# Performance work log

Hardware: AMD Instinct MI355X
Metric: run time of the kernel (lower is better)

The kernel has to match this reference:

```python
import jax, jax.numpy as jnp
import numpy as np
import math

D_MODEL = 2048
N_HEADS = 16
D_FF = 8192
SEQ = 2048
BATCH = 2
THETA = 10000.0
EPS = 1e-5


def _rope(x, pos):
    # x: [B, H, S, d_k] ; pos: [B, S] int
    d = x.shape[-1]
    inv_freq = 1.0 / (THETA ** (jnp.arange(0, d, 2, dtype=jnp.float32) / d))  # [d/2]
    ang = pos[..., None].astype(jnp.float32) * inv_freq  # [B, S, d/2]
    cos = jnp.cos(ang)[:, None, :, :, None]  # [B,1,S,d/2,1]
    sin = jnp.sin(ang)[:, None, :, :, None]
    xr = x.reshape(*x.shape[:-1], d // 2, 2)
    x1, x2 = xr[..., 0], xr[..., 1]
    rot = jnp.stack((-x2, x1), axis=-1)  # rotate pairs
    out = xr * cos + rot * sin
    return out.reshape(x.shape)


def _trunc_normal(key, shape, in_f, out_f):
    std = math.sqrt(2.0 / (in_f + out_f))
    return jax.random.truncated_normal(key, -3.0, 3.0, shape, jnp.float32) * std


def setup_inputs() -> dict:
    key = jax.random.key(0)
    ks = jax.random.split(key, 8)
    x = jax.random.normal(ks[0], (BATCH, SEQ, D_MODEL), jnp.float32)
    token_positions = jnp.sort(jax.random.randint(ks[1], (BATCH, SEQ), 0, SEQ), axis=-1)
    W_qkv = _trunc_normal(ks[2], (3 * D_MODEL, D_MODEL), D_MODEL, 3 * D_MODEL)
    W_o = _trunc_normal(ks[3], (D_MODEL, D_MODEL), D_MODEL, D_MODEL)
    W1 = _trunc_normal(ks[4], (D_FF, D_MODEL), D_MODEL, D_FF)
    W3 = _trunc_normal(ks[5], (D_FF, D_MODEL), D_MODEL, D_FF)
    W2 = _trunc_normal(ks[6], (D_MODEL, D_FF), D_FF, D_MODEL)
    g1 = jnp.ones((D_MODEL,), jnp.float32)
    g2 = jnp.ones((D_MODEL,), jnp.float32)
    return {"x": x, "token_positions": token_positions, "W_qkv": W_qkv, "W_o": W_o,
            "g1": g1, "g2": g2, "W1": W1, "W3": W3, "W2": W2}


def _rmsnorm(x, g):
    xf = x.astype(jnp.float32)
    rms = jnp.sqrt(jnp.mean(xf * xf, axis=-1, keepdims=True) + EPS)
    return (xf / rms * g).astype(x.dtype)


def reference(x, token_positions, W_qkv, W_o, g1, g2, W1, W3, W2):
    B, S, D = x.shape
    H = N_HEADS
    dk = D // H
    # --- attention sublayer ---
    h = _rmsnorm(x, g1)
    qkv = jnp.einsum('bsi,oi->bso', h, W_qkv)  # [B,S,3D]
    q, k, v = jnp.split(qkv, 3, axis=-1)
    to_heads = lambda t: t.reshape(B, S, H, dk).transpose(0, 2, 1, 3)  # [B,H,S,dk]
    q, k, v = to_heads(q), to_heads(k), to_heads(v)
    q = _rope(q, token_positions)
    k = _rope(k, token_positions)
    scores = jnp.einsum('bhnd,bhmd->bhnm', q, k) / math.sqrt(dk)  # [B,H,S,S]
    mask = jnp.tril(jnp.ones((S, S), dtype=bool))
    scores = jnp.where(mask, scores, -jnp.inf)
    attn = jax.nn.softmax(scores, axis=-1)
    o = jnp.einsum('bhnm,bhmd->bhnd', attn, v)
    o = o.transpose(0, 2, 1, 3).reshape(B, S, D)
    x = x + jnp.einsum('bsi,oi->bso', o, W_o)
    # --- SwiGLU FFN sublayer ---
    h2 = _rmsnorm(x, g2)
    x1 = jnp.einsum('bsi,oi->bso', h2, W1)
    x3 = jnp.einsum('bsi,oi->bso', h2, W3)
    x = x + jnp.einsum('bsi,oi->bso', jax.nn.silu(x1) * x3, W2)
    return x
```

## Files before the change

### kernel.cpp

```cpp
#include <hip/hip_runtime.h>

#define DEV __device__ __forceinline__

typedef __bf16 bf16x8 __attribute__((ext_vector_type(8)));
typedef float f32x4 __attribute__((ext_vector_type(4)));
typedef unsigned short u16x8 __attribute__((ext_vector_type(8)));

DEV unsigned short f2bf(float f) {
  unsigned int u = __float_as_uint(f);
  u += 0x7fffu + ((u >> 16) & 1u);
  return (unsigned short)(u >> 16);
}
DEV float bf2f(unsigned short h) {
  return __uint_as_float(((unsigned int)h) << 16);
}
DEV void gload16(const void* g, void* l) {
  __builtin_amdgcn_global_load_lds(
      (const __attribute__((address_space(1))) unsigned int*)g,
      (__attribute__((address_space(3))) unsigned int*)l, 16, 0, 0);
}
DEV f32x4 mfma16(bf16x8 a, bf16x8 b, f32x4 c) {
  return __builtin_amdgcn_mfma_f32_16x16x32_bf16(a, b, c, 0, 0, 0);
}

#define SB   __builtin_amdgcn_s_barrier()
#define SCH  __builtin_amdgcn_sched_barrier(0)
#define LGKM0 asm volatile("s_waitcnt lgkmcnt(0)" ::: "memory")
#define LGKM4 asm volatile("s_waitcnt lgkmcnt(4)" ::: "memory")
#define VM6  asm volatile("s_waitcnt vmcnt(6)" ::: "memory")
#define PRIO1 __builtin_amdgcn_s_setprio(1)
#define PRIO0 __builtin_amdgcn_s_setprio(0)

__global__ __launch_bounds__(256) void k_cvt(const float* __restrict__ in,
                                             unsigned short* __restrict__ out, int n8) {
  const int stride = gridDim.x * 256;
  for (int i = blockIdx.x * 256 + threadIdx.x; i < n8; i += stride) {
    const float4* p = (const float4*)(in + (long)i * 8);
    const float4 a = p[0], b = p[1];
    u16x8 o = { f2bf(a.x), f2bf(a.y), f2bf(a.z), f2bf(a.w),
                f2bf(b.x), f2bf(b.y), f2bf(b.z), f2bf(b.w) };
    *(u16x8*)(out + (long)i * 8) = o;
  }
}

__global__ __launch_bounds__(256) void k_add(float* __restrict__ out,
                                             const float* __restrict__ p, int n4) {
  const int stride = gridDim.x * 256;
  for (int i = blockIdx.x * 256 + threadIdx.x; i < n4; i += stride) {
    float4 a = ((const float4*)out)[i];
    const float4 b = ((const float4*)p)[i];
    a.x += b.x; a.y += b.y; a.z += b.z; a.w += b.w;
    ((float4*)out)[i] = a;
  }
}

__global__ __launch_bounds__(256) void k_rmsnorm(const float* __restrict__ x,
                                                 const float* __restrict__ g,
                                                 unsigned short* __restrict__ out) {
  const int row = blockIdx.x;
  const int t = threadIdx.x;
  const float4* xr = (const float4*)(x + (long)row * 2048);
  const float4 a = xr[t * 2], c = xr[t * 2 + 1];
  float ss = a.x * a.x + a.y * a.y + a.z * a.z + a.w * a.w +
             c.x * c.x + c.y * c.y + c.z * c.z + c.w * c.w;
#pragma unroll
  for (int o = 32; o > 0; o >>= 1) ss += __shfl_down(ss, o);
  __shared__ float ws4[4];
  __shared__ float invs;
  if ((t & 63) == 0) ws4[t >> 6] = ss;
  __syncthreads();
  if (t == 0) invs = 1.0f / sqrtf((ws4[0] + ws4[1] + ws4[2] + ws4[3]) * (1.0f / 2048.0f) + 1e-5f);
  __syncthreads();
  const float inv = invs;
  const float4* gr = (const float4*)g;
  const float4 g0 = gr[t * 2], g1v = gr[t * 2 + 1];
  u16x8 o8 = { f2bf(a.x * inv * g0.x),  f2bf(a.y * inv * g0.y),
               f2bf(a.z * inv * g0.z),  f2bf(a.w * inv * g0.w),
               f2bf(c.x * inv * g1v.x), f2bf(c.y * inv * g1v.y),
               f2bf(c.z * inv * g1v.z), f2bf(c.w * inv * g1v.w) };
  *(u16x8*)(out + (long)row * 2048 + t * 8) = o8;
}

__global__ __launch_bounds__(256) void k_rmsnorm2(const float* __restrict__ xa,
                                                  const float* __restrict__ xb,
                                                  const float* __restrict__ g,
                                                  float* __restrict__ xsum,
                                                  unsigned short* __restrict__ out) {
  const int row = blockIdx.x;
  const int t = threadIdx.x;
  const float4* ar = (const float4*)(xa + (long)row * 2048);
  const float4* br = (const float4*)(xb + (long)row * 2048);
  float4 a = ar[t * 2], c = ar[t * 2 + 1];
  const float4 pa = br[t * 2], pc = br[t * 2 + 1];
  a.x += pa.x; a.y += pa.y; a.z += pa.z; a.w += pa.w;
  c.x += pc.x; c.y += pc.y; c.z += pc.z; c.w += pc.w;
  float4* sr = (float4*)(xsum + (long)row * 2048);
  sr[t * 2] = a; sr[t * 2 + 1] = c;
  float ss = a.x * a.x + a.y * a.y + a.z * a.z + a.w * a.w +
             c.x * c.x + c.y * c.y + c.z * c.z + c.w * c.w;
#pragma unroll
  for (int o = 32; o > 0; o >>= 1) ss += __shfl_down(ss, o);
  __shared__ float ws4[4];
  __shared__ float invs;
  if ((t & 63) == 0) ws4[t >> 6] = ss;
  __syncthreads();
  if (t == 0) invs = 1.0f / sqrtf((ws4[0] + ws4[1] + ws4[2] + ws4[3]) * (1.0f / 2048.0f) + 1e-5f);
  __syncthreads();
  const float inv = invs;
  const float4* gr = (const float4*)g;
  const float4 g0 = gr[t * 2], g1v = gr[t * 2 + 1];
  u16x8 o8 = { f2bf(a.x * inv * g0.x),  f2bf(a.y * inv * g0.y),
               f2bf(a.z * inv * g0.z),  f2bf(a.w * inv * g0.w),
               f2bf(c.x * inv * g1v.x), f2bf(c.y * inv * g1v.y),
               f2bf(c.z * inv * g1v.z), f2bf(c.w * inv * g1v.w) };
  *(u16x8*)(out + (long)row * 2048 + t * 8) = o8;
}

template <int EPI>
__global__ __launch_bounds__(512, 2) void k_gemm256(
    const unsigned short* __restrict__ A, const unsigned short* __restrict__ B,
    unsigned short* __restrict__ outBF, float* __restrict__ outF,
    const float* __restrict__ resid, const unsigned short* __restrict__ aux,
    float* __restrict__ partial, const int* __restrict__ tp,
    unsigned short* __restrict__ p2, unsigned short* __restrict__ p3,
    int M, int N, int K, int Keff) {
  __shared__ __align__(16) unsigned short lds[2][2][2][128][64];
  const int tid = threadIdx.x;
  const int wid = tid >> 6, lane = tid & 63;
  const int wr = wid >> 2, wc = wid & 3;
  const int fr = lane & 15, g4 = lane >> 4;

  const int nwg = gridDim.x;
  int bid = blockIdx.x;
  { int q = nwg >> 3, r = nwg & 7, xcd = bid & 7, lo = bid >> 3;
    bid = (xcd < r ? xcd * (q + 1) : r * (q + 1) + (xcd - r) * q) + lo; }
  int tile = bid, ks = 0;
  if constexpr (EPI == 3) { ks = bid & 1; tile = bid >> 1; }
  const int nxb = N >> 8;
  const int bx = tile % nxb, by = tile / nxb;
  const int arow0 = by << 8, bcol0 = bx << 8;
  const int NT = Keff >> 6;

  const int srow = tid >> 3;
  const int sg = (tid & 7) ^ (srow & 7);
  const unsigned short* Asrc = A + (long)(arow0 + srow) * K + (long)ks * Keff + (sg << 3);
  const unsigned short* Bsrc = B + (long)(bcol0 + srow) * K + (long)ks * Keff + (sg << 3);

  const int posk0 = (g4 ^ (lane & 7)) << 3;
  const int posk1 = ((4 + g4) ^ (lane & 7)) << 3;

  f32x4 acc[8][4] = {};
  bf16x8 a[4][2], b0[2][2], b1[2][2];

#define STAGE(SRC, xs, bufi, mat, h)                                            \
  { const unsigned short* s_ = (SRC) + (long)(h) * 128 * K + (long)(xs) * 64;   \
    unsigned short* d_ = &lds[bufi][mat][h][0][0] + wid * 512;                  \
    gload16(s_, d_);                                                            \
    gload16(s_ + (long)64 * K, d_ + 4096); }
#define RD_A(BA, mh)                                                            \
  _Pragma("unroll") for (int m_ = 0; m_ < 4; ++m_) {                            \
    const unsigned short* p_ = (BA) + ((mh) * 64 + m_ * 16 + fr) * 64;          \
    a[m_][0] = *(const bf16x8*)(p_ + posk0);                                    \
    a[m_][1] = *(const bf16x8*)(p_ + posk1); }
#define RD_B(BB, arr, nh)                                                       \
  _Pragma("unroll") for (int n_ = 0; n_ < 2; ++n_) {                            \
    const unsigned short* p_ = (BB) + ((nh) * 32 + n_ * 16 + fr) * 64;          \
    arr[n_][0] = *(const bf16x8*)(p_ + posk0);                                  \
    arr[n_][1] = *(const bf16x8*)(p_ + posk1); }
#define MM(mh, nh, Bv)                                                          \
  _Pragma("unroll") for (int k_ = 0; k_ < 2; ++k_)                              \
  _Pragma("unroll") for (int m_ = 0; m_ < 4; ++m_)                              \
  _Pragma("unroll") for (int n_ = 0; n_ < 2; ++n_)                              \
    acc[(mh)*4+m_][(nh)*2+n_] = mfma16(a[m_][k_], Bv[n_][k_], acc[(mh)*4+m_][(nh)*2+n_]);

  STAGE(Asrc, 0, 0, 0, 0);
  STAGE(Asrc, 0, 0, 0, 1);
  STAGE(Bsrc, 0, 0, 1, 0);
  STAGE(Bsrc, 0, 0, 1, 1);
  { const int x1p = (NT > 1) ? 1 : 0;
    STAGE(Bsrc, x1p, 1, 1, 0);
    STAGE(Bsrc, x1p, 1, 1, 1);
    STAGE(Asrc, x1p, 1, 0, 0); }
  VM6; SCH; SB; SCH;
  {
    const unsigned short* baseA = &lds[0][0][wr][0][0];
    const unsigned short* baseB = &lds[0][1][wc >> 1][0][0] + (wc & 1) * 4096;
    RD_A(baseA, 0); RD_B(baseB, b0, 0);
  }

  for (int t = 0; t < NT; ++t) {
    const unsigned short* baseA = &lds[t & 1][0][wr][0][0];
    const unsigned short* baseB = &lds[t & 1][1][wc >> 1][0][0] + (wc & 1) * 4096;
    const unsigned short* baseA2 = &lds[(t + 1) & 1][0][wr][0][0];
    const unsigned short* baseB2 = &lds[(t + 1) & 1][1][wc >> 1][0][0] + (wc & 1) * 4096;
    const int x1 = (t + 1 < NT) ? t + 1 : NT - 1;
    const int x2i = (t + 2 < NT) ? t + 2 : NT - 1;
    const int bn = (t + 1) & 1, bc = t & 1;

    SB;
    RD_B(baseB, b1, 1);
    STAGE(Asrc, x1, bn, 0, 1);
    LGKM4; SCH;
    PRIO1; MM(0, 0, b0); PRIO0;
    LGKM0; SCH;
    PRIO1; MM(0, 1, b1); PRIO0;

    SB;
    RD_A(baseA, 1);
    STAGE(Bsrc, x2i, bc, 1, 0);
    LGKM0; SCH;
    PRIO1; MM(1, 1, b1); PRIO0;

    SB;
    STAGE(Asrc, x2i, bc, 0, 0);
    STAGE(Bsrc, x2i, bc, 1, 1);
    PRIO1; MM(1, 0, b0); PRIO0;
    VM6; SCH; SB; SCH;
    RD_A(baseA2, 0);
    RD_B(baseB2, b0, 0);
  }
#undef STAGE
#undef RD_A
#undef RD_B
#undef MM

  const int er = g4 << 2;
  if constexpr (EPI == 4) {
    const int region = bcol0 >> 11;
#pragma unroll
    for (int m = 0; m < 8; ++m) {
      const int grow = arow0 + wr * 128 + m * 16 + er;
      float pos4[4];
#pragma unroll
      for (int r = 0; r < 4; ++r)
        pos4[r] = (region < 2) ? (float)tp[grow + r] : 0.f;
#pragma unroll
      for (int n = 0; n < 4; ++n) {
        const int gcol = bcol0 + wc * 64 + n * 16 + fr;
        const int d = gcol & 127;
        const float invf = __expf((float)(d >> 1) * -0.14391156831212787f);
        const int h = (gcol >> 7) & 15;
#pragma unroll
        for (int r = 0; r < 4; ++r) {
          const int row = grow + r;
          const int b = row >> 11, s = row & 2047;
          float v = acc[m][n][r];
          if (region < 2) {
            const float other = __shfl_xor(v, 1);
            float cc, sn;
            __sincosf(pos4[r] * invf, &sn, &cc);
            v = (d & 1) ? (v * cc + other * sn) : (v * cc - other * sn);
          }
          unsigned short* dst = (region == 0) ? outBF : (region == 1 ? p2 : p3);
          dst[((long)((b << 4) + h) * 2048 + s) * 128 + d] = f2bf(v);
        }
      }
    }
  } else {
#pragma unroll
    for (int m = 0; m < 8; ++m) {
#pragma unroll
      for (int n = 0; n < 4; ++n) {
        const int grow = arow0 + wr * 128 + m * 16 + er;
        const int gcol = bcol0 + wc * 64 + n * 16 + fr;
#pragma unroll
        for (int r = 0; r < 4; ++r) {
          const long idx = (long)(grow + r) * N + gcol;
          const float v = acc[m][n][r];
          if constexpr (EPI == 0) {
            outBF[idx] = f2bf(v);
          } else if constexpr (EPI == 1) {
            outF[idx] = resid[idx] + v;
          } else if constexpr (EPI == 2) {
            const float x1v = bf2f(aux[idx]);
            const float sl = x1v / (1.0f + __expf(-x1v));
            outBF[idx] = f2bf(sl * v);
          } else {
            if (ks == 0) outF[idx] = resid[idx] + v;
            else         partial[idx] = v;
          }
        }
      }
    }
  }
}

__global__ __launch_bounds__(256) void k_vtrans(const unsigned short* __restrict__ Vh,
                                                unsigned short* __restrict__ Vt, int S) {
  __shared__ __align__(16) unsigned short t[128 * 72];
  const int bh = blockIdx.x;
  const int s0 = blockIdx.y << 6;
  const int tid = threadIdx.x;
  const int sl = tid >> 2, c4 = tid & 3;
#pragma unroll
  for (int it = 0; it < 4; ++it) {
    const int chunk = c4 * 4 + it;
    u16x8 v = *(const u16x8*)(Vh + ((long)bh * S + s0 + sl) * 128 + chunk * 8);
#pragma unroll
    for (int jj = 0; jj < 8; ++jj) t[(chunk * 8 + jj) * 72 + sl] = v[jj];
  }
  __syncthreads();
  const int d = tid >> 1, half = tid & 1;
  unsigned short* dst = Vt + ((long)bh * 128 + d) * S + s0 + half * 32;
  const unsigned short* srcr = &t[d * 72 + half * 32];
#pragma unroll
  for (int u = 0; u < 4; ++u)
    *(u16x8*)(dst + u * 8) = *(const u16x8*)(srcr + u * 8);
}

__global__ __launch_bounds__(256) void k_attn(const unsigned short* __restrict__ Q,
                                              const unsigned short* __restrict__ Kh,
                                              const unsigned short* __restrict__ Vt,
                                              unsigned short* __restrict__ O, int S) {
  __shared__ __align__(16) unsigned short lds_k[64 * 128];
  __shared__ __align__(16) unsigned short lds_v[128 * 64];
  __shared__ __align__(16) unsigned short lds_p[4 * 16 * 64];
  const int bh = blockIdx.x;
  const int b = bh >> 4, h = bh & 15;
  const int qt = gridDim.y - 1 - blockIdx.y;
  const int q0 = qt << 6;
  const int tid = threadIdx.x, w = tid >> 6, lane = tid & 63;
  const int fr = lane & 15, g4 = lane >> 4;

  bf16x8 qf[4];
  {
    const unsigned short* qb = Q + ((long)bh * S + q0 + w * 16 + fr) * 128 + (g4 << 3);
#pragma unroll
    for (int kk = 0; kk < 4; ++kk) qf[kk] = *(const bf16x8*)(qb + kk * 32);
  }

  f32x4 accO[8] = {};
  float mrow[4], lrow[4];
#pragma unroll
  for (int r = 0; r < 4; ++r) { mrow[r] = -1e30f; lrow[r] = 0.f; }

  const int k_row = (w << 4) + g4;
  const int k_cb = fr << 4;
  const int v_row = (w << 5) + (lane >> 3);
  const int v_cb = (lane & 7) << 4;
  const long kbase = (long)bh * S * 128;
  const long vbase = (long)bh * 128 * S;

  const int ntile = qt + 1;
  for (int it = 0; it < ntile; ++it) {
    const int kv0 = it << 6;
#pragma unroll
    for (int j = 0; j < 4; ++j) {
      const int kr = k_row + j * 4;
      const int kc = k_cb ^ ((kr & 7) << 4);
      gload16(Kh + kbase + (long)(kv0 + kr) * 128 + (kc >> 1), &lds_k[w * 2048 + j * 512]);
      const int vr = v_row + j * 8;
      const int vc = v_cb ^ ((vr & 7) << 4);
      gload16(Vt + vbase + (long)vr * S + kv0 + (vc >> 1), &lds_v[w * 2048 + j * 512]);
    }
    __syncthreads();

    f32x4 sc[4] = {};
#pragma unroll
    for (int kk = 0; kk < 4; ++kk) {
      const int kb = (kk << 6) + (g4 << 4);
#pragma unroll
      for (int n = 0; n < 4; ++n) {
        const int krw = n * 16 + fr;
        const int swz = (krw & 7) << 4;
        bf16x8 kf = *(const bf16x8*)&lds_k[krw * 128 + ((kb ^ swz) >> 1)];
        sc[n] = mfma16(qf[kk], kf, sc[n]);
      }
    }

    const float scl = 0.08838834764831845f;
    float sv[4][4];
    const bool needmask = (kv0 + 63 > q0 + w * 16);
#pragma unroll
    for (int n = 0; n < 4; ++n)
#pragma unroll
      for (int r = 0; r < 4; ++r) {
        float v = sc[n][r] * scl;
        if (needmask) {
          const int qi = q0 + w * 16 + (g4 << 2) + r;
          const int ki = kv0 + n * 16 + fr;
          if (ki > qi) v = -1e30f;
        }
        sv[n][r] = v;
      }
    float corr[4];
#pragma unroll
    for (int r = 0; r < 4; ++r) {
      float tm = fmaxf(fmaxf(sv[0][r], sv[1][r]), fmaxf(sv[2][r], sv[3][r]));
      tm = fmaxf(tm, __shfl_xor(tm, 1));
      tm = fmaxf(tm, __shfl_xor(tm, 2));
      tm = fmaxf(tm, __shfl_xor(tm, 4));
      tm = fmaxf(tm, __shfl_xor(tm, 8));
      const float mn = fmaxf(mrow[r], tm);
      corr[r] = __expf(mrow[r] - mn);
      mrow[r] = mn;
    }
    float rs[4] = {0.f, 0.f, 0.f, 0.f};
#pragma unroll
    for (int n = 0; n < 4; ++n)
#pragma unroll
      for (int r = 0; r < 4; ++r) {
        const float p = __expf(sv[n][r] - mrow[r]);
        rs[r] += p;
        const int pr = (g4 << 2) + r;
        const int pc = (n * 16 + fr) << 1;
        lds_p[(w << 10) + pr * 64 + ((pc ^ ((pr & 7) << 4)) >> 1)] = f2bf(p);
      }
#pragma unroll
    for (int r = 0; r < 4; ++r) {
      float s = rs[r];
      s += __shfl_xor(s, 1);
      s += __shfl_xor(s, 2);
      s += __shfl_xor(s, 4);
      s += __shfl_xor(s, 8);
      lrow[r] = lrow[r] * corr[r] + s;
    }
#pragma unroll
    for (int cb = 0; cb < 8; ++cb)
#pragma unroll
      for (int r = 0; r < 4; ++r) accO[cb][r] *= corr[r];

#pragma unroll
    for (int kk = 0; kk < 2; ++kk) {
      const int pb = (kk << 6) + (g4 << 4);
      bf16x8 pf = *(const bf16x8*)&lds_p[(w << 10) + fr * 64 + ((pb ^ ((fr & 7) << 4)) >> 1)];
#pragma unroll
      for (int cb = 0; cb < 8; ++cb) {
        const int vrw = cb * 16 + fr;
        bf16x8 vf = *(const bf16x8*)&lds_v[vrw * 64 + ((pb ^ ((vrw & 7) << 4)) >> 1)];
        accO[cb] = mfma16(pf, vf, accO[cb]);
      }
    }
    __syncthreads();
  }

#pragma unroll
  for (int cb = 0; cb < 8; ++cb)
#pragma unroll
    for (int r = 0; r < 4; ++r) {
      const int si = q0 + w * 16 + (g4 << 2) + r;
      const float o = accO[cb][r] / lrow[r];
      O[((long)b * S + si) * 2048 + h * 128 + cb * 16 + fr] = f2bf(o);
    }
}

extern "C" void kernel_launch(void* const* d_in, const int* in_sizes, int n_in,
                              void* d_out, int out_size, void* d_ws, size_t ws_size,
                              hipStream_t stream) {
  const float* x    = (const float*)d_in[0];
  const int*   tp   = (const int*)d_in[1];
  const float* Wqkv = (const float*)d_in[2];
  const float* Wo   = (const float*)d_in[3];
  const float* g1   = (const float*)d_in[4];
  const float* g2   = (const float*)d_in[5];
  const float* W1   = (const float*)d_in[6];
  const float* W3   = (const float*)d_in[7];
  const float* W2   = (const float*)d_in[8];
  float* out = (float*)d_out;

  char* ws = (char*)d_ws;
  const size_t MB = 1024 * 1024;
  unsigned short* Qh      = (unsigned short*)(ws + 0 * MB);
  unsigned short* Kh      = (unsigned short*)(ws + 16 * MB);
  unsigned short* Vt      = (unsigned short*)(ws + 32 * MB);
  unsigned short* Vh      = (unsigned short*)(ws + 48 * MB);
  unsigned short* O_bf    = (unsigned short*)(ws + 48 * MB);
  unsigned short* t_bf    = (unsigned short*)(ws + 0 * MB);
  float*          x2      = (float*)         (ws + 64 * MB);
  unsigned short* h2_bf   = (unsigned short*)(ws + 96 * MB);
  unsigned short* wo_bf   = (unsigned short*)(ws + 96 * MB);
  unsigned short* wqkv_bf = (unsigned short*)(ws + 112 * MB);
  unsigned short* w1_bf   = (unsigned short*)(ws + 112 * MB);
  unsigned short* w2_bf   = (unsigned short*)(ws + 112 * MB);
  unsigned short* h1_bf   = (unsigned short*)(ws + 144 * MB);
  float*          part    = (float*)         (ws + 144 * MB);
  unsigned short* w3_bf   = (unsigned short*)(ws + 144 * MB);

  const int S = 2048;

  k_cvt<<<1024, 256, 0, stream>>>(Wqkv, wqkv_bf, 12582912 / 8);
  k_rmsnorm<<<4096, 256, 0, stream>>>(x, g1, h1_bf);
  k_gemm256<4><<<dim3(384), 512, 0, stream>>>(h1_bf, wqkv_bf, Qh, nullptr, nullptr, nullptr,
                                              nullptr, tp, Kh, Vh, 4096, 6144, 2048, 2048);
  k_vtrans<<<dim3(32, 32), 256, 0, stream>>>(Vh, Vt, S);
  k_cvt<<<1024, 256, 0, stream>>>(Wo, wo_bf, 4194304 / 8);
  k_cvt<<<1024, 256, 0, stream>>>(W1, w1_bf, 16777216 / 8);
  k_attn<<<dim3(32, 32), 256, 0, stream>>>(Qh, Kh, Vt, O_bf, S);
  k_gemm256<3><<<dim3(256), 512, 0, stream>>>(O_bf, wo_bf, nullptr, x2, x, nullptr,
                                              part, nullptr, nullptr, nullptr, 4096, 2048, 2048, 1024);

  k_rmsnorm2<<<4096, 256, 0, stream>>>(x2, part, g2, x2, h2_bf);
  k_cvt<<<1024, 256, 0, stream>>>(W3, w3_bf, 16777216 / 8);
  k_gemm256<0><<<dim3(512), 512, 0, stream>>>(h2_bf, w1_bf, t_bf, nullptr, nullptr, nullptr,
                                              nullptr, nullptr, nullptr, nullptr, 4096, 8192, 2048, 2048);
  k_cvt<<<1024, 256, 0, stream>>>(W2, w2_bf, 16777216 / 8);
  k_gemm256<2><<<dim3(512), 512, 0, stream>>>(h2_bf, w3_bf, t_bf, nullptr, nullptr, t_bf,
                                              nullptr, nullptr, nullptr, nullptr, 4096, 8192, 2048, 2048);
  k_gemm256<3><<<dim3(256), 512, 0, stream>>>(t_bf, w2_bf, nullptr, out, x2, nullptr,
                                              part, nullptr, nullptr, nullptr, 4096, 2048, 8192, 4096);
  k_add<<<2048, 256, 0, stream>>>(out, part, 2097152);
}
```

Before: 807.2 us.

## Replace split-K down-projection GEMM with 256x128-tile kernel and drop partial add

The final FFN down-projection (K=8192) used a 256x256-tile GEMM with split-K=2, writing a partial buffer that a separate add kernel then summed. This switches to a new 256x128-tile GEMM with triple-buffered LDS and no K split, so 256 workgroups still fill the device. The residual add is fused into its epilogue. This removes the partial-buffer write/read and one kernel launch, at the cost of lower per-tile arithmetic intensity and a longer per-workgroup K loop.

```diff
diff --git a/kernel.cpp b/kernel.cpp
--- a/kernel.cpp
+++ b/kernel.cpp
@@ -40,17 +40,6 @@
     u16x8 o = { f2bf(a.x), f2bf(a.y), f2bf(a.z), f2bf(a.w),
                 f2bf(b.x), f2bf(b.y), f2bf(b.z), f2bf(b.w) };
     *(u16x8*)(out + (long)i * 8) = o;
-  }
-}
-
-__global__ __launch_bounds__(256) void k_add(float* __restrict__ out,
-                                             const float* __restrict__ p, int n4) {
-  const int stride = gridDim.x * 256;
-  for (int i = blockIdx.x * 256 + threadIdx.x; i < n4; i += stride) {
-    float4 a = ((const float4*)out)[i];
-    const float4 b = ((const float4*)p)[i];
-    a.x += b.x; a.y += b.y; a.z += b.z; a.w += b.w;
-    ((float4*)out)[i] = a;
   }
 }
 
@@ -285,6 +274,104 @@
   }
 }
 
+__global__ __launch_bounds__(512, 1) void k_gemm_n128(
+    const unsigned short* __restrict__ A, const unsigned short* __restrict__ B,
+    float* __restrict__ outF, const float* __restrict__ resid, int M, int N, int K) {
+  __shared__ __align__(16) unsigned short lds[3][384 * 64];
+  const int tid = threadIdx.x;
+  const int wid = tid >> 6, lane = tid & 63;
+  const int wr = wid >> 1, wc = wid & 1;
+  const int fr = lane & 15, g4 = lane >> 4;
+
+  const int nwg = gridDim.x;
+  int bid = blockIdx.x;
+  { int q = nwg >> 3, r = nwg & 7, xcd = bid & 7, lo = bid >> 3;
+    bid = (xcd < r ? xcd * (q + 1) : r * (q + 1) + (xcd - r) * q) + lo; }
+  const int nxb = N >> 7;
+  const int bx = bid % nxb, by = bid / nxb;
+  const int arow0 = by << 8, bcol0 = bx << 7;
+  const int NT = K >> 6;
+
+  const int srow = tid >> 3;
+  const int sg = (tid & 7) ^ (srow & 7);
+  const unsigned short* Asrc = A + (long)(arow0 + srow) * K + (sg << 3);
+  const unsigned short* Bsrc = B + (long)(bcol0 + srow) * K + (sg << 3);
+
+  const int posk0 = (g4 ^ (lane & 7)) << 3;
+  const int posk1 = ((4 + g4) ^ (lane & 7)) << 3;
+
+  f32x4 acc[4][4] = {};
+  bf16x8 a[4][2], bl[2][2], bh[2][2];
+
+#define SITE_A(xs, bufi, s)                                                    \
+  gload16(Asrc + (long)((s) * 64) * K + (long)(xs) * 64,                       \
+          &lds[bufi][(s) * 4096] + wid * 512);
+#define SITE_B(xs, bufi, s)                                                    \
+  gload16(Bsrc + (long)((s) * 64) * K + (long)(xs) * 64,                       \
+          &lds[bufi][16384 + (s) * 4096] + wid * 512);
+#define RDA(BUF)                                                               \
+  _Pragma("unroll") for (int m_ = 0; m_ < 4; ++m_) {                           \
+    const unsigned short* p_ = (BUF) + (wr * 64 + m_ * 16 + fr) * 64;          \
+    a[m_][0] = *(const bf16x8*)(p_ + posk0);                                   \
+    a[m_][1] = *(const bf16x8*)(p_ + posk1); }
+#define RDB(BUF, arr, off)                                                     \
+  _Pragma("unroll") for (int n_ = 0; n_ < 2; ++n_) {                           \
+    const unsigned short* p_ = (BUF) + 16384 + (wc * 64 + (off) + n_ * 16 + fr) * 64; \
+    arr[n_][0] = *(const bf16x8*)(p_ + posk0);                                 \
+    arr[n_][1] = *(const bf16x8*)(p_ + posk1); }
+#define MMN(nh, Bv)                                                            \
+  _Pragma("unroll") for (int k_ = 0; k_ < 2; ++k_)                             \
+  _Pragma("unroll") for (int m_ = 0; m_ < 4; ++m_)                             \
+  _Pragma("unroll") for (int n_ = 0; n_ < 2; ++n_)                             \
+    acc[m_][(nh)*2+n_] = mfma16(a[m_][k_], Bv[n_][k_], acc[m_][(nh)*2+n_]);
+
+  SITE_A(0, 0, 0); SITE_A(0, 0, 1); SITE_A(0, 0, 2); SITE_A(0, 0, 3);
+  SITE_B(0, 0, 0); SITE_B(0, 0, 1);
+  { const int x1p = (NT > 1) ? 1 : 0;
+    SITE_A(x1p, 1, 0); SITE_A(x1p, 1, 1); SITE_A(x1p, 1, 2); SITE_A(x1p, 1, 3);
+    SITE_B(x1p, 1, 0); SITE_B(x1p, 1, 1); }
+  VM6; SCH; SB; SCH;
+  RDA(lds[0]); RDB(lds[0], bl, 0);
+
+  for (int t = 0; t < NT; ++t) {
+    const unsigned short* bufb = lds[t % 3];
+    const unsigned short* bufn = lds[(t + 1) % 3];
+    const int bn = (t + 2) % 3;
+    const int xs = (t + 2 < NT) ? t + 2 : NT - 1;
+
+    SB;
+    RDB(bufb, bh, 32);
+    SITE_A(xs, bn, 0); SITE_A(xs, bn, 1);
+    LGKM4; SCH;
+    PRIO1; MMN(0, bl); PRIO0;
+    SITE_A(xs, bn, 2); SITE_A(xs, bn, 3); SITE_B(xs, bn, 0); SITE_B(xs, bn, 1);
+    LGKM0; SCH;
+    PRIO1; MMN(1, bh); PRIO0;
+    VM6; SCH; SB; SCH;
+    RDA(bufn); RDB(bufn, bl, 0);
+  }
+#undef SITE_A
+#undef SITE_B
+#undef RDA
+#undef RDB
+#undef MMN
+
+  const int er = g4 << 2;
+#pragma unroll
+  for (int m = 0; m < 4; ++m) {
+#pragma unroll
+    for (int n = 0; n < 4; ++n) {
+      const int grow = arow0 + wr * 64 + m * 16 + er;
+      const int gcol = bcol0 + wc * 64 + n * 16 + fr;
+#pragma unroll
+      for (int r = 0; r < 4; ++r) {
+        const long idx = (long)(grow + r) * N + gcol;
+        outF[idx] = resid[idx] + acc[m][n][r];
+      }
+    }
+  }
+}
+
 __global__ __launch_bounds__(256) void k_vtrans(const unsigned short* __restrict__ Vh,
                                                 unsigned short* __restrict__ Vt, int S) {
   __shared__ __align__(16) unsigned short t[128 * 72];
@@ -496,7 +583,5 @@
   k_cvt<<<1024, 256, 0, stream>>>(W2, w2_bf, 16777216 / 8);
   k_gemm256<2><<<dim3(512), 512, 0, stream>>>(h2_bf, w3_bf, t_bf, nullptr, nullptr, t_bf,
                                               nullptr, nullptr, nullptr, nullptr, 4096, 8192, 2048, 2048);
-  k_gemm256<3><<<dim3(256), 512, 0, stream>>>(t_bf, w2_bf, nullptr, out, x2, nullptr,
-                                              part, nullptr, nullptr, nullptr, 4096, 2048, 8192, 4096);
-  k_add<<<2048, 256, 0, stream>>>(out, part, 2097152);
-}
+  k_gemm_n128<<<dim3(256), 512, 0, stream>>>(t_bf, w2_bf, out, x2, 4096, 2048, 8192);
+}
```

Result: faster. 765.8 us (-5.1%).
